# Performance work log

Measured on AMD Instinct MI355X. Metric: run time of the kernel, lower is better.

The kernel has to match this reference:

```python
import jax, jax.numpy as jnp
import numpy as np

D_MODEL = 768
N_HEADS = 4
D_HEAD = D_MODEL // N_HEADS
EPS = 1e-3  # keras LayerNormalization default


def gelu_tanh(x):
    return 0.5 * x * (1.0 + jnp.tanh(np.sqrt(2.0 / np.pi) * (x + 0.044715 * x ** 3)))


def layer_norm(x, g, b):
    mu = jnp.mean(x, axis=-1, keepdims=True)
    var = jnp.mean(jnp.square(x - mu), axis=-1, keepdims=True)
    return (x - mu) * jax.lax.rsqrt(var + EPS) * g + b


def setup_inputs() -> dict:
    key = jax.random.key(0)
    ks = jax.random.split(key, 12)
    B, S = 8, 1024
    x = jax.random.normal(ks[0], (B, S, D_MODEL), dtype=jnp.float32)
    # causal mask: 1 on strictly-future positions (added as mask * -1e9)
    mask = jnp.triu(jnp.ones((S, S), dtype=jnp.float32), k=1)[None, None]
    s = 0.02
    params = {
        'W1': jax.random.normal(ks[1], (D_MODEL, 3 * D_MODEL)) * s,
        'b1': jnp.zeros((3 * D_MODEL,), jnp.float32),
        'W3': jax.random.normal(ks[2], (D_MODEL, D_MODEL)) * s,
        'b3': jnp.zeros((D_MODEL,), jnp.float32),
        'W2': jax.random.normal(ks[3], (D_MODEL, 4 * D_MODEL)) * s,
        'b2': jnp.zeros((4 * D_MODEL,), jnp.float32),
        'W4': jax.random.normal(ks[4], (4 * D_MODEL, D_MODEL)) * s,
        'b4': jnp.zeros((D_MODEL,), jnp.float32),
        'g1': jnp.ones((D_MODEL,), jnp.float32),
        'be1': jnp.zeros((D_MODEL,), jnp.float32),
        'g2': jnp.ones((D_MODEL,), jnp.float32),
        'be2': jnp.zeros((D_MODEL,), jnp.float32),
    }
    return {'x': x, 'mask': mask, **params}


def reference(x, mask, W1, b1, W3, b3, W2, b2, W4, b4, g1, be1, g2, be2):
    B, S, _ = x.shape
    xn = layer_norm(x, g1, be1)
    qkv = xn @ W1 + b1                                  # [B,S,3D]
    q, k, v = jnp.split(qkv, 3, axis=-1)
    def split_heads(t):
        return t.reshape(B, S, N_HEADS, D_HEAD).transpose(0, 2, 1, 3)  # [B,H,S,dh]
    q, k, v = map(split_heads, (q, k, v))
    present = jnp.stack([k, v], axis=1)                  # [B,2,H,S,dh]
    w = jnp.einsum('bhqd,bhkd->bhqk', q, k)
    # NOTE: source divides by rsqrt(d_head) => multiplies by sqrt(d_head) (faithful bug)
    w = w * jnp.sqrt(jnp.float32(D_HEAD))
    w = w + mask * -1e9
    w = jax.nn.softmax(w, axis=-1)
    attn = jnp.einsum('bhqk,bhkd->bhqd', w, v)           # [B,H,S,dh]
    attn = attn.transpose(0, 2, 1, 3).reshape(B, S, D_MODEL)
    x = attn @ W3 + b3 + x                               # residual 1
    xn2 = layer_norm(x, g2, be2)
    h = gelu_tanh(xn2 @ W2 + b2)                         # [B,S,4D]
    x = h @ W4 + b4 + x                                  # residual 2
    return x, present
```

## Files before the change

### kernel.cpp

```cpp
#include <hip/hip_runtime.h>
#include <hip/hip_bf16.h>
#include <cstdint>

#define D_MODEL 768
#define NH 4
#define DH 192
#define SEQ 1024
#define BATCH 8

typedef __bf16 bf16x8 __attribute__((ext_vector_type(8)));
typedef float floatx4 __attribute__((ext_vector_type(4)));

__device__ __forceinline__ float bf2f(ushort u) {
    union { uint32_t i; float f; } x; x.i = ((uint32_t)u) << 16; return x.f;
}
__device__ __forceinline__ ushort f2bf(float f) {
    union { float f; uint32_t i; } x; x.f = f;
    uint32_t i = x.i;
    uint32_t r = (i + 0x7FFFu + ((i >> 16) & 1u)) >> 16;
    return (ushort)r;
}

template <int SPLIT>
__global__ void ln_kernel(const float* __restrict__ x, const float* __restrict__ g,
                          const float* __restrict__ be,
                          ushort* __restrict__ y_hi, ushort* __restrict__ y_lo) {
    int row = blockIdx.x;
    int tid = threadIdx.x;
    const float* xr = x + (size_t)row * D_MODEL;
    float v[3];
    float s = 0.f, ss = 0.f;
#pragma unroll
    for (int i = 0; i < 3; i++) {
        float t = xr[tid + i * 256];
        v[i] = t; s += t; ss += t * t;
    }
#pragma unroll
    for (int off = 32; off > 0; off >>= 1) {
        s += __shfl_down(s, off);
        ss += __shfl_down(ss, off);
    }
    __shared__ float rs[4], rss[4];
    int wid = tid >> 6;
    if ((tid & 63) == 0) { rs[wid] = s; rss[wid] = ss; }
    __syncthreads();
    s = rs[0] + rs[1] + rs[2] + rs[3];
    ss = rss[0] + rss[1] + rss[2] + rss[3];
    float mu = s * (1.f / 768.f);
    float var = ss * (1.f / 768.f) - mu * mu;
    float rstd = rsqrtf(var + 1e-3f);
#pragma unroll
    for (int i = 0; i < 3; i++) {
        int d = tid + i * 256;
        float val = (v[i] - mu) * rstd * g[d] + be[d];
        ushort hi = f2bf(val);
        y_hi[(size_t)row * D_MODEL + d] = hi;
        if (SPLIT) y_lo[(size_t)row * D_MODEL + d] = f2bf(val - bf2f(hi));
    }
}

__global__ void transpose_kernel(const float* __restrict__ W, ushort* __restrict__ Wt,
                                 int K, int N) {
    __shared__ ushort tile[64][65];
    int nt = N >> 6;
    int bk = blockIdx.x / nt, bn = blockIdx.x % nt;
    int tid = threadIdx.x;
#pragma unroll
    for (int i = 0; i < 16; i++) {
        int lin = i * 256 + tid; int r = lin >> 6, c = lin & 63;
        tile[r][c] = f2bf(W[(size_t)(bk * 64 + r) * N + bn * 64 + c]);
    }
    __syncthreads();
#pragma unroll
    for (int i = 0; i < 16; i++) {
        int lin = i * 256 + tid; int r = lin >> 6, c = lin & 63;
        Wt[(size_t)(bn * 64 + r) * K + bk * 64 + c] = tile[c][r];
    }
}

__global__ void transpose_split_kernel(const float* __restrict__ W,
                                       ushort* __restrict__ Wt_hi, ushort* __restrict__ Wt_lo,
                                       int K, int N) {
    __shared__ ushort th[64][65];
    __shared__ ushort tl[64][65];
    int nt = N >> 6;
    int bk = blockIdx.x / nt, bn = blockIdx.x % nt;
    int tid = threadIdx.x;
#pragma unroll
    for (int i = 0; i < 16; i++) {
        int lin = i * 256 + tid; int r = lin >> 6, c = lin & 63;
        float v = W[(size_t)(bk * 64 + r) * N + bn * 64 + c];
        ushort hi = f2bf(v);
        th[r][c] = hi;
        tl[r][c] = f2bf(v - bf2f(hi));
    }
    __syncthreads();
#pragma unroll
    for (int i = 0; i < 16; i++) {
        int lin = i * 256 + tid; int r = lin >> 6, c = lin & 63;
        size_t o = (size_t)(bn * 64 + r) * K + bk * 64 + c;
        Wt_hi[o] = th[c][r];
        Wt_lo[o] = tl[c][r];
    }
}

__global__ void transpose_v_kernel(const float* __restrict__ qkv, ushort* __restrict__ Vtg) {
    __shared__ ushort tile[64][65];
    int bi = blockIdx.x;
    int dt = bi % 12;
    int st = (bi / 12) % 16;
    int b  = bi / 192;
    int tid = threadIdx.x;
#pragma unroll
    for (int i = 0; i < 16; i++) {
        int lin = i * 256 + tid; int r = lin >> 6, c = lin & 63;
        tile[r][c] = f2bf(qkv[(size_t)(b * 1024 + st * 64 + r) * 2304 + 1536 + dt * 64 + c]);
    }
    __syncthreads();
#pragma unroll
    for (int i = 0; i < 16; i++) {
        int lin = i * 256 + tid; int r = lin >> 6, c = lin & 63;
        Vtg[(size_t)(b * 768 + dt * 64 + r) * 1024 + st * 64 + c] = tile[c][r];
    }
}

__global__ __launch_bounds__(256, 2) void gemm_qkv_split(
    const ushort* __restrict__ Ah, const ushort* __restrict__ Al,
    const ushort* __restrict__ Bh, const ushort* __restrict__ Bl,
    const float* __restrict__ bias, float* __restrict__ Cout, int M, int N, int K) {
    __shared__ __align__(16) __bf16 sAh[128][48];
    __shared__ __align__(16) __bf16 sAl[128][48];
    __shared__ __align__(16) __bf16 sBh[128][48];
    __shared__ __align__(16) __bf16 sBl[128][48];
    int tid = threadIdx.x;
    int rowBase = blockIdx.y << 7;
    int colBase = blockIdx.x << 7;
    int wave = tid >> 6, lane = tid & 63;
    int wm = (wave & 1) << 6, wn = (wave >> 1) << 6;
    int lrow = lane & 15, lk = (lane >> 4) << 3;
    floatx4 acc[4][4] = {};

    int lr = tid >> 2;
    int lc = (tid & 3) << 3;
    size_t aoff = (size_t)(rowBase + lr) * K + lc;
    size_t boff = (size_t)(colBase + lr) * K + lc;

    for (int k0 = 0; k0 < K; k0 += 32) {
        uint4 ah0 = *(const uint4*)(Ah + aoff + k0);
        uint4 ah1 = *(const uint4*)(Ah + aoff + (size_t)64 * K + k0);
        uint4 al0 = *(const uint4*)(Al + aoff + k0);
        uint4 al1 = *(const uint4*)(Al + aoff + (size_t)64 * K + k0);
        uint4 bh0 = *(const uint4*)(Bh + boff + k0);
        uint4 bh1 = *(const uint4*)(Bh + boff + (size_t)64 * K + k0);
        uint4 bl0 = *(const uint4*)(Bl + boff + k0);
        uint4 bl1 = *(const uint4*)(Bl + boff + (size_t)64 * K + k0);
        *(uint4*)&sAh[lr][lc] = ah0;  *(uint4*)&sAh[lr + 64][lc] = ah1;
        *(uint4*)&sAl[lr][lc] = al0;  *(uint4*)&sAl[lr + 64][lc] = al1;
        *(uint4*)&sBh[lr][lc] = bh0;  *(uint4*)&sBh[lr + 64][lc] = bh1;
        *(uint4*)&sBl[lr][lc] = bl0;  *(uint4*)&sBl[lr + 64][lc] = bl1;
        __syncthreads();
        bf16x8 afh[4], afl[4], bvh[4], bvl[4];
#pragma unroll
        for (int i = 0; i < 4; i++) {
            afh[i] = *(const bf16x8*)&sAh[wm + i * 16 + lrow][lk];
            afl[i] = *(const bf16x8*)&sAl[wm + i * 16 + lrow][lk];
        }
#pragma unroll
        for (int jj = 0; jj < 4; jj++) {
            bvh[jj] = *(const bf16x8*)&sBh[wn + jj * 16 + lrow][lk];
            bvl[jj] = *(const bf16x8*)&sBl[wn + jj * 16 + lrow][lk];
        }
#pragma unroll
        for (int i = 0; i < 4; i++)
#pragma unroll
            for (int jj = 0; jj < 4; jj++) {
                acc[i][jj] = __builtin_amdgcn_mfma_f32_16x16x32_bf16(afh[i], bvh[jj], acc[i][jj], 0, 0, 0);
                acc[i][jj] = __builtin_amdgcn_mfma_f32_16x16x32_bf16(afh[i], bvl[jj], acc[i][jj], 0, 0, 0);
                acc[i][jj] = __builtin_amdgcn_mfma_f32_16x16x32_bf16(afl[i], bvh[jj], acc[i][jj], 0, 0, 0);
            }
        __syncthreads();
    }
    int cr = (lane >> 4) << 2;
    int cc = lane & 15;
#pragma unroll
    for (int jj = 0; jj < 4; jj++) {
        int col = colBase + wn + jj * 16 + cc;
        float bvs = bias[col];
#pragma unroll
        for (int i = 0; i < 4; i++) {
            int row0 = rowBase + wm + i * 16 + cr;
#pragma unroll
            for (int r = 0; r < 4; r++)
                Cout[(size_t)(row0 + r) * N + col] = acc[i][jj][r] + bvs;
        }
    }
}

template <int GELU, int RES, int OUTF32>
__global__ __launch_bounds__(256, 2) void gemm_bt(
    const ushort* __restrict__ A, const ushort* __restrict__ Bt,
    const float* __restrict__ bias, const float* __restrict__ resid,
    void* __restrict__ Cout, int M, int N, int K) {
    __shared__ __align__(16) __bf16 sA[128][48];
    __shared__ __align__(16) __bf16 sB[128][48];
    int tid = threadIdx.x;
    int rowBase = blockIdx.y << 7;
    int colBase = blockIdx.x << 7;
    int wave = tid >> 6, lane = tid & 63;
    int wm = (wave & 1) << 6, wn = (wave >> 1) << 6;
    int lrow = lane & 15, lk = (lane >> 4) << 3;
    floatx4 acc[4][4] = {};

    int lr = tid >> 2;
    int lc = (tid & 3) << 3;
    const ushort* Ab = A + (size_t)(rowBase + lr) * K + lc;
    const ushort* Bb = Bt + (size_t)(colBase + lr) * K + lc;

    for (int k0 = 0; k0 < K; k0 += 32) {
        uint4 a0 = *(const uint4*)(Ab + k0);
        uint4 a1 = *(const uint4*)(Ab + (size_t)64 * K + k0);
        uint4 b0 = *(const uint4*)(Bb + k0);
        uint4 b1 = *(const uint4*)(Bb + (size_t)64 * K + k0);
        *(uint4*)&sA[lr][lc] = a0;
        *(uint4*)&sA[lr + 64][lc] = a1;
        *(uint4*)&sB[lr][lc] = b0;
        *(uint4*)&sB[lr + 64][lc] = b1;
        __syncthreads();
        bf16x8 af[4], bv[4];
#pragma unroll
        for (int i = 0; i < 4; i++) af[i] = *(const bf16x8*)&sA[wm + i * 16 + lrow][lk];
#pragma unroll
        for (int jj = 0; jj < 4; jj++) bv[jj] = *(const bf16x8*)&sB[wn + jj * 16 + lrow][lk];
#pragma unroll
        for (int i = 0; i < 4; i++)
#pragma unroll
            for (int jj = 0; jj < 4; jj++)
                acc[i][jj] = __builtin_amdgcn_mfma_f32_16x16x32_bf16(af[i], bv[jj], acc[i][jj], 0, 0, 0);
        __syncthreads();
    }
    int cr = (lane >> 4) << 2;
    int cc = lane & 15;
#pragma unroll
    for (int jj = 0; jj < 4; jj++) {
        int col = colBase + wn + jj * 16 + cc;
        float bvs = bias[col];
#pragma unroll
        for (int i = 0; i < 4; i++) {
            int row0 = rowBase + wm + i * 16 + cr;
#pragma unroll
            for (int r = 0; r < 4; r++) {
                int row = row0 + r;
                float v = acc[i][jj][r] + bvs;
                if (GELU) {
                    float u = v;
                    v = 0.5f * u * (1.f + tanhf(0.7978845608028654f * (u + 0.044715f * u * u * u)));
                }
                if (RES) v += resid[(size_t)row * N + col];
                if (OUTF32) ((float*)Cout)[(size_t)row * N + col] = v;
                else ((ushort*)Cout)[(size_t)row * N + col] = f2bf(v);
            }
        }
    }
}

__global__ void split_kernel(const float* __restrict__ qkv, float* __restrict__ present,
                             ushort* __restrict__ Khg, ushort* __restrict__ Klg) {
    int tok = blockIdx.x;
    int tid = threadIdx.x;
    int b = tok >> 10, s = tok & 1023;
    const float* src = qkv + (size_t)tok * 2304 + 768;
#pragma unroll
    for (int i = 0; i < 6; i++) {
        int c = tid + i * 256;
        float v = src[c];
        int kv = (c >= 768) ? 1 : 0;
        int within = c - kv * 768;
        int h = within / DH;
        int d = within - h * DH;
        size_t idx = ((size_t)(((b * 2 + kv) * NH + h) * SEQ + s)) * DH + d;
        present[idx] = v;
        if (!kv) {
            ushort hi = f2bf(v);
            Khg[(size_t)tok * 768 + c] = hi;
            Klg[(size_t)tok * 768 + c] = f2bf(v - bf2f(hi));
        }
    }
}

__global__ __launch_bounds__(512, 2) void attn_flash(
    const float* __restrict__ qkv, const ushort* __restrict__ Khg,
    const ushort* __restrict__ Klg, const ushort* __restrict__ Vtg,
    ushort* __restrict__ attn2) {
    int bi = blockIdx.x;
    int j = bi & 7;
    int h = (bi >> 3) & 3;
    int b = bi >> 5;
    int tid = threadIdx.x;
    int wave = tid >> 6, lane = tid & 63;
    int l15 = lane & 15, quad = lane >> 4;
    int tile = (wave < 4) ? (15 - j) : j;
    int w16 = wave & 3;
    int s0 = tile << 6;
    int its = 2 * (15 - j) + 2;
    int myKt = (s0 + w16 * 16 + 15) >> 5;

    __shared__ __align__(16) __bf16 sKh[2][32][200];
    __shared__ __align__(16) __bf16 sKl[2][32][200];
    __shared__ __align__(16) __bf16 sVt[2][192][40];
    __shared__ __align__(16) ushort sP[8][16][40];

    const bool lo_half = (tid < 256);
    const int kr0 = tid / 24, ke0 = (tid % 24) * 8;
    const int c1 = lo_half ? (512 + tid) : (256 + tid);
    const int kr1 = c1 / 24, ke1 = (c1 % 24) * 8;
    const int vd0 = tid >> 2, ve0 = (tid & 3) * 8;
    const int vd1 = (512 + tid) >> 2, ve1 = ((512 + tid) & 3) * 8;

    const ushort* Khb = Khg + (size_t)(b * 1024) * 768 + h * 192;
    const ushort* Klb = Klg + (size_t)(b * 1024) * 768 + h * 192;
    const ushort* Vtb = Vtg + ((size_t)(b * 768) + h * 192) * 1024;
    const ushort* Bb = lo_half ? Khb : Klb;
    __bf16* pKB = lo_half ? &sKh[0][kr1][ke1] : &sKl[0][kr1][ke1];

    uint4 rA, rB, rC, rD, rE;

    rA = *(const uint4*)(Khb + (size_t)kr0 * 768 + ke0);
    rC = *(const uint4*)(Klb + (size_t)kr0 * 768 + ke0);
    rB = *(const uint4*)(Bb + (size_t)kr1 * 768 + ke1);
    rD = *(const uint4*)(Vtb + (size_t)vd0 * 1024 + ve0);
    if (lo_half) rE = *(const uint4*)(Vtb + (size_t)vd1 * 1024 + ve1);

    bf16x8 qh[6], ql[6];
    {
        int qrow = s0 + w16 * 16 + l15;
        const float* qp = qkv + (size_t)(b * SEQ + qrow) * 2304 + h * DH + quad * 8;
#pragma unroll
        for (int dt = 0; dt < 6; dt++) {
            float4 v0 = *(const float4*)(qp + dt * 32);
            float4 v1 = *(const float4*)(qp + dt * 32 + 4);
            float vv[8] = {v0.x, v0.y, v0.z, v0.w, v1.x, v1.y, v1.z, v1.w};
            bf16x8 hh, ll;
#pragma unroll
            for (int jj = 0; jj < 8; jj++) {
                float sv = vv[jj] * 13.856406460551018f;
                ushort hu = f2bf(sv);
                ((ushort*)&hh)[jj] = hu;
                ((ushort*)&ll)[jj] = f2bf(sv - bf2f(hu));
            }
            qh[dt] = hh; ql[dt] = ll;
        }
    }

    floatx4 O[12] = {};
    float m_run[4], l_run[4];
#pragma unroll
    for (int r = 0; r < 4; r++) { m_run[r] = -1e30f; l_run[r] = 0.f; }

    *(uint4*)&sKh[0][kr0][ke0] = rA;
    *(uint4*)&sKl[0][kr0][ke0] = rC;
    *(uint4*)(pKB) = rB;
    *(uint4*)&sVt[0][vd0][ve0] = rD;
    if (lo_half) *(uint4*)&sVt[0][vd1][ve1] = rE;
    __syncthreads();

    for (int kt = 0; kt < its; kt++) {
        int cur = kt & 1;
        bool pfetch = (kt + 1 < its);
        if (pfetch) {
            int koff = (kt + 1) * 32;
            rA = *(const uint4*)(Khb + (size_t)(koff + kr0) * 768 + ke0);
            rC = *(const uint4*)(Klb + (size_t)(koff + kr0) * 768 + ke0);
            rB = *(const uint4*)(Bb + (size_t)(koff + kr1) * 768 + ke1);
            rD = *(const uint4*)(Vtb + (size_t)vd0 * 1024 + koff + ve0);
            if (lo_half) rE = *(const uint4*)(Vtb + (size_t)vd1 * 1024 + koff + ve1);
        }
        if (kt <= myKt) {
            floatx4 S0 = {}, S1 = {};
#pragma unroll
            for (int dt = 0; dt < 6; dt++) {
                bf16x8 k0h = *(const bf16x8*)&sKh[cur][l15][dt * 32 + quad * 8];
                bf16x8 k0l = *(const bf16x8*)&sKl[cur][l15][dt * 32 + quad * 8];
                bf16x8 k1h = *(const bf16x8*)&sKh[cur][16 + l15][dt * 32 + quad * 8];
                bf16x8 k1l = *(const bf16x8*)&sKl[cur][16 + l15][dt * 32 + quad * 8];
                S0 = __builtin_amdgcn_mfma_f32_16x16x32_bf16(qh[dt], k0h, S0, 0, 0, 0);
                S0 = __builtin_amdgcn_mfma_f32_16x16x32_bf16(qh[dt], k0l, S0, 0, 0, 0);
                S0 = __builtin_amdgcn_mfma_f32_16x16x32_bf16(ql[dt], k0h, S0, 0, 0, 0);
                S1 = __builtin_amdgcn_mfma_f32_16x16x32_bf16(qh[dt], k1h, S1, 0, 0, 0);
                S1 = __builtin_amdgcn_mfma_f32_16x16x32_bf16(qh[dt], k1l, S1, 0, 0, 0);
                S1 = __builtin_amdgcn_mfma_f32_16x16x32_bf16(ql[dt], k1h, S1, 0, 0, 0);
            }
            int qg = s0 + w16 * 16 + quad * 4;
            int colb = kt * 32 + l15;
            float mt[4];
#pragma unroll
            for (int r = 0; r < 4; r++) {
                float a = (colb <= qg + r) ? S0[r] : -1e30f;
                float c = (colb + 16 <= qg + r) ? S1[r] : -1e30f;
                S0[r] = a; S1[r] = c;
                mt[r] = fmaxf(a, c);
            }
#pragma unroll
            for (int m = 1; m <= 8; m <<= 1)
#pragma unroll
                for (int r = 0; r < 4; r++) mt[r] = fmaxf(mt[r], __shfl_xor(mt[r], m));
            float alpha[4], rsum[4], P0[4], P1[4];
#pragma unroll
            for (int r = 0; r < 4; r++) {
                float mn = fmaxf(m_run[r], mt[r]);
                alpha[r] = __expf(m_run[r] - mn);
                m_run[r] = mn;
                P0[r] = __expf(S0[r] - mn);
                P1[r] = __expf(S1[r] - mn);
                rsum[r] = P0[r] + P1[r];
            }
#pragma unroll
            for (int m = 1; m <= 8; m <<= 1)
#pragma unroll
                for (int r = 0; r < 4; r++) rsum[r] += __shfl_xor(rsum[r], m);
#pragma unroll
            for (int r = 0; r < 4; r++) l_run[r] = l_run[r] * alpha[r] + rsum[r];
#pragma unroll
            for (int t = 0; t < 12; t++)
#pragma unroll
                for (int r = 0; r < 4; r++) O[t][r] *= alpha[r];
#pragma unroll
            for (int r = 0; r < 4; r++) {
                sP[wave][quad * 4 + r][l15]      = f2bf(P0[r]);
                sP[wave][quad * 4 + r][16 + l15] = f2bf(P1[r]);
            }
            bf16x8 pfrag = *(const bf16x8*)&sP[wave][l15][quad * 8];
#pragma unroll
            for (int t = 0; t < 12; t++) {
                bf16x8 vf = *(const bf16x8*)&sVt[cur][t * 16 + l15][quad * 8];
                O[t] = __builtin_amdgcn_mfma_f32_16x16x32_bf16(pfrag, vf, O[t], 0, 0, 0);
            }
        }
        if (pfetch) {
            int nb = cur ^ 1;
            *(uint4*)&sKh[nb][kr0][ke0] = rA;
            *(uint4*)&sKl[nb][kr0][ke0] = rC;
            *(uint4*)(pKB + nb * 6400) = rB;
            *(uint4*)&sVt[nb][vd0][ve0] = rD;
            if (lo_half) *(uint4*)&sVt[nb][vd1][ve1] = rE;
        }
        __syncthreads();
    }

    float inv[4];
#pragma unroll
    for (int r = 0; r < 4; r++) inv[r] = 1.f / l_run[r];
    int qrow = s0 + w16 * 16 + quad * 4;
#pragma unroll
    for (int t = 0; t < 12; t++)
#pragma unroll
        for (int r = 0; r < 4; r++)
            attn2[(size_t)(b * SEQ + qrow + r) * D_MODEL + h * DH + t * 16 + l15] =
                f2bf(O[t][r] * inv[r]);
}

extern "C" void kernel_launch(void* const* d_in, const int* in_sizes, int n_in,
                              void* d_out, int out_size, void* d_ws, size_t ws_size,
                              hipStream_t stream) {
    const float* x  = (const float*)d_in[0];
    const float* W1 = (const float*)d_in[2];
    const float* b1 = (const float*)d_in[3];
    const float* W3 = (const float*)d_in[4];
    const float* b3 = (const float*)d_in[5];
    const float* W2 = (const float*)d_in[6];
    const float* b2 = (const float*)d_in[7];
    const float* W4 = (const float*)d_in[8];
    const float* b4 = (const float*)d_in[9];
    const float* g1 = (const float*)d_in[10];
    const float* be1 = (const float*)d_in[11];
    const float* g2 = (const float*)d_in[12];
    const float* be2 = (const float*)d_in[13];

    char* ws = (char*)d_ws;
    ushort* W1t_hi = (ushort*)(ws + 0);
    ushort* W1t_lo = (ushort*)(ws + 3538944);
    ushort* W3t    = (ushort*)(ws + 7077888);
    ushort* W2t    = (ushort*)(ws + 8257536);
    ushort* W4t    = (ushort*)(ws + 12976128);
    ushort* xn_hi  = (ushort*)(ws + 17694720);
    ushort* attn2  = (ushort*)(ws + 17694720);
    ushort* xn_lo  = (ushort*)(ws + 30277632);
    ushort* Khg    = (ushort*)(ws + 30277632);
    ushort* xn2    = (ushort*)(ws + 30277632);
    float*  x1     = (float*)(ws + 42860544);
    ushort* Klg    = (ushort*)(ws + 42860544);
    ushort* Vtg    = (ushort*)(ws + 55443456);
    float*  qkvf   = (float*)(ws + 68026368);
    ushort* hbuf   = (ushort*)(ws + 68026368);

    float* out0 = (float*)d_out;
    float* present = out0 + 6291456;

    transpose_split_kernel<<<(768 / 64) * (2304 / 64), 256, 0, stream>>>(W1, W1t_hi, W1t_lo, 768, 2304);
    transpose_kernel<<<(768 / 64) * (768 / 64), 256, 0, stream>>>(W3, W3t, 768, 768);
    transpose_kernel<<<(768 / 64) * (3072 / 64), 256, 0, stream>>>(W2, W2t, 768, 3072);
    transpose_kernel<<<(3072 / 64) * (768 / 64), 256, 0, stream>>>(W4, W4t, 3072, 768);

    ln_kernel<1><<<8192, 256, 0, stream>>>(x, g1, be1, xn_hi, xn_lo);
    gemm_qkv_split<<<dim3(2304 / 128, 8192 / 128), 256, 0, stream>>>(
        xn_hi, xn_lo, W1t_hi, W1t_lo, b1, qkvf, 8192, 2304, 768);
    split_kernel<<<8192, 256, 0, stream>>>(qkvf, present, Khg, Klg);
    transpose_v_kernel<<<1536, 256, 0, stream>>>(qkvf, Vtg);
    attn_flash<<<BATCH * NH * 8, 512, 0, stream>>>(qkvf, Khg, Klg, Vtg, attn2);
    gemm_bt<0, 1, 1><<<dim3(768 / 128, 8192 / 128), 256, 0, stream>>>(
        attn2, W3t, b3, x, x1, 8192, 768, 768);
    ln_kernel<0><<<8192, 256, 0, stream>>>(x1, g2, be2, xn2, nullptr);
    gemm_bt<1, 0, 0><<<dim3(3072 / 128, 8192 / 128), 256, 0, stream>>>(
        xn2, W2t, b2, nullptr, hbuf, 8192, 3072, 768);
    gemm_bt<0, 1, 1><<<dim3(768 / 128, 8192 / 128), 256, 0, stream>>>(
        hbuf, W4t, b4, x1, out0, 8192, 768, 3072);
}
```

Baseline: 527.4 us.

## Prefetch next K tile into registers and double-buffer LDS in GEMM kernels

Both GEMM kernels now load the next K-slice from global memory into registers before running the MFMAs on the current slice, so load latency overlaps compute. gemm_bt double-buffers its shared tiles and needs only one barrier per iteration, while gemm_qkv_split keeps a single buffer with two barriers. LDS row padding drops from 48 to 40 elements, gemm_bt's launch bounds rise to 3 blocks per CU, and GELU is rewritten as u/(1+exp(-2z)) using the fast __expf. The risks are extra register pressure under the tighter occupancy bound and small numeric differences from the fast exp.

```diff
diff --git a/kernel.cpp b/kernel.cpp
--- a/kernel.cpp
+++ b/kernel.cpp
@@ -128,10 +128,10 @@
     const ushort* __restrict__ Ah, const ushort* __restrict__ Al,
     const ushort* __restrict__ Bh, const ushort* __restrict__ Bl,
     const float* __restrict__ bias, float* __restrict__ Cout, int M, int N, int K) {
-    __shared__ __align__(16) __bf16 sAh[128][48];
-    __shared__ __align__(16) __bf16 sAl[128][48];
-    __shared__ __align__(16) __bf16 sBh[128][48];
-    __shared__ __align__(16) __bf16 sBl[128][48];
+    __shared__ __align__(16) __bf16 sAh[128][40];
+    __shared__ __align__(16) __bf16 sAl[128][40];
+    __shared__ __align__(16) __bf16 sBh[128][40];
+    __shared__ __align__(16) __bf16 sBl[128][40];
     int tid = threadIdx.x;
     int rowBase = blockIdx.y << 7;
     int colBase = blockIdx.x << 7;
@@ -145,20 +145,37 @@
     size_t aoff = (size_t)(rowBase + lr) * K + lc;
     size_t boff = (size_t)(colBase + lr) * K + lc;
 
-    for (int k0 = 0; k0 < K; k0 += 32) {
-        uint4 ah0 = *(const uint4*)(Ah + aoff + k0);
-        uint4 ah1 = *(const uint4*)(Ah + aoff + (size_t)64 * K + k0);
-        uint4 al0 = *(const uint4*)(Al + aoff + k0);
-        uint4 al1 = *(const uint4*)(Al + aoff + (size_t)64 * K + k0);
-        uint4 bh0 = *(const uint4*)(Bh + boff + k0);
-        uint4 bh1 = *(const uint4*)(Bh + boff + (size_t)64 * K + k0);
-        uint4 bl0 = *(const uint4*)(Bl + boff + k0);
-        uint4 bl1 = *(const uint4*)(Bl + boff + (size_t)64 * K + k0);
+    {
+        uint4 ah0 = *(const uint4*)(Ah + aoff);
+        uint4 ah1 = *(const uint4*)(Ah + aoff + (size_t)64 * K);
+        uint4 al0 = *(const uint4*)(Al + aoff);
+        uint4 al1 = *(const uint4*)(Al + aoff + (size_t)64 * K);
+        uint4 bh0 = *(const uint4*)(Bh + boff);
+        uint4 bh1 = *(const uint4*)(Bh + boff + (size_t)64 * K);
+        uint4 bl0 = *(const uint4*)(Bl + boff);
+        uint4 bl1 = *(const uint4*)(Bl + boff + (size_t)64 * K);
         *(uint4*)&sAh[lr][lc] = ah0;  *(uint4*)&sAh[lr + 64][lc] = ah1;
         *(uint4*)&sAl[lr][lc] = al0;  *(uint4*)&sAl[lr + 64][lc] = al1;
         *(uint4*)&sBh[lr][lc] = bh0;  *(uint4*)&sBh[lr + 64][lc] = bh1;
         *(uint4*)&sBl[lr][lc] = bl0;  *(uint4*)&sBl[lr + 64][lc] = bl1;
-        __syncthreads();
+    }
+    __syncthreads();
+
+    int nt = K >> 5;
+    for (int t = 0; t < nt; t++) {
+        bool pf = (t + 1 < nt);
+        uint4 ah0, ah1, al0, al1, bh0, bh1, bl0, bl1;
+        if (pf) {
+            int k0 = (t + 1) << 5;
+            ah0 = *(const uint4*)(Ah + aoff + k0);
+            ah1 = *(const uint4*)(Ah + aoff + (size_t)64 * K + k0);
+            al0 = *(const uint4*)(Al + aoff + k0);
+            al1 = *(const uint4*)(Al + aoff + (size_t)64 * K + k0);
+            bh0 = *(const uint4*)(Bh + boff + k0);
+            bh1 = *(const uint4*)(Bh + boff + (size_t)64 * K + k0);
+            bl0 = *(const uint4*)(Bl + boff + k0);
+            bl1 = *(const uint4*)(Bl + boff + (size_t)64 * K + k0);
+        }
         bf16x8 afh[4], afl[4], bvh[4], bvl[4];
 #pragma unroll
         for (int i = 0; i < 4; i++) {
@@ -178,7 +195,14 @@
                 acc[i][jj] = __builtin_amdgcn_mfma_f32_16x16x32_bf16(afh[i], bvl[jj], acc[i][jj], 0, 0, 0);
                 acc[i][jj] = __builtin_amdgcn_mfma_f32_16x16x32_bf16(afl[i], bvh[jj], acc[i][jj], 0, 0, 0);
             }
-        __syncthreads();
+        if (pf) {
+            __syncthreads();
+            *(uint4*)&sAh[lr][lc] = ah0;  *(uint4*)&sAh[lr + 64][lc] = ah1;
+            *(uint4*)&sAl[lr][lc] = al0;  *(uint4*)&sAl[lr + 64][lc] = al1;
+            *(uint4*)&sBh[lr][lc] = bh0;  *(uint4*)&sBh[lr + 64][lc] = bh1;
+            *(uint4*)&sBl[lr][lc] = bl0;  *(uint4*)&sBl[lr + 64][lc] = bl1;
+            __syncthreads();
+        }
     }
     int cr = (lane >> 4) << 2;
     int cc = lane & 15;
@@ -197,12 +221,12 @@
 }
 
 template <int GELU, int RES, int OUTF32>
-__global__ __launch_bounds__(256, 2) void gemm_bt(
+__global__ __launch_bounds__(256, 3) void gemm_bt(
     const ushort* __restrict__ A, const ushort* __restrict__ Bt,
     const float* __restrict__ bias, const float* __restrict__ resid,
     void* __restrict__ Cout, int M, int N, int K) {
-    __shared__ __align__(16) __bf16 sA[128][48];
-    __shared__ __align__(16) __bf16 sB[128][48];
+    __shared__ __align__(16) __bf16 sA[2][128][40];
+    __shared__ __align__(16) __bf16 sB[2][128][40];
     int tid = threadIdx.x;
     int rowBase = blockIdx.y << 7;
     int colBase = blockIdx.x << 7;
@@ -216,26 +240,47 @@
     const ushort* Ab = A + (size_t)(rowBase + lr) * K + lc;
     const ushort* Bb = Bt + (size_t)(colBase + lr) * K + lc;
 
-    for (int k0 = 0; k0 < K; k0 += 32) {
-        uint4 a0 = *(const uint4*)(Ab + k0);
-        uint4 a1 = *(const uint4*)(Ab + (size_t)64 * K + k0);
-        uint4 b0 = *(const uint4*)(Bb + k0);
-        uint4 b1 = *(const uint4*)(Bb + (size_t)64 * K + k0);
-        *(uint4*)&sA[lr][lc] = a0;
-        *(uint4*)&sA[lr + 64][lc] = a1;
-        *(uint4*)&sB[lr][lc] = b0;
-        *(uint4*)&sB[lr + 64][lc] = b1;
-        __syncthreads();
+    {
+        uint4 a0 = *(const uint4*)(Ab);
+        uint4 a1 = *(const uint4*)(Ab + (size_t)64 * K);
+        uint4 b0 = *(const uint4*)(Bb);
+        uint4 b1 = *(const uint4*)(Bb + (size_t)64 * K);
+        *(uint4*)&sA[0][lr][lc] = a0;
+        *(uint4*)&sA[0][lr + 64][lc] = a1;
+        *(uint4*)&sB[0][lr][lc] = b0;
+        *(uint4*)&sB[0][lr + 64][lc] = b1;
+    }
+    __syncthreads();
+
+    int nt = K >> 5;
+    for (int t = 0; t < nt; t++) {
+        int cur = t & 1;
+        bool pf = (t + 1 < nt);
+        uint4 a0, a1, b0, b1;
+        if (pf) {
+            int k0 = (t + 1) << 5;
+            a0 = *(const uint4*)(Ab + k0);
+            a1 = *(const uint4*)(Ab + (size_t)64 * K + k0);
+            b0 = *(const uint4*)(Bb + k0);
+            b1 = *(const uint4*)(Bb + (size_t)64 * K + k0);
+        }
         bf16x8 af[4], bv[4];
 #pragma unroll
-        for (int i = 0; i < 4; i++) af[i] = *(const bf16x8*)&sA[wm + i * 16 + lrow][lk];
-#pragma unroll
-        for (int jj = 0; jj < 4; jj++) bv[jj] = *(const bf16x8*)&sB[wn + jj * 16 + lrow][lk];
+        for (int i = 0; i < 4; i++) af[i] = *(const bf16x8*)&sA[cur][wm + i * 16 + lrow][lk];
+#pragma unroll
+        for (int jj = 0; jj < 4; jj++) bv[jj] = *(const bf16x8*)&sB[cur][wn + jj * 16 + lrow][lk];
 #pragma unroll
         for (int i = 0; i < 4; i++)
 #pragma unroll
             for (int jj = 0; jj < 4; jj++)
                 acc[i][jj] = __builtin_amdgcn_mfma_f32_16x16x32_bf16(af[i], bv[jj], acc[i][jj], 0, 0, 0);
+        if (pf) {
+            int nb = cur ^ 1;
+            *(uint4*)&sA[nb][lr][lc] = a0;
+            *(uint4*)&sA[nb][lr + 64][lc] = a1;
+            *(uint4*)&sB[nb][lr][lc] = b0;
+            *(uint4*)&sB[nb][lr + 64][lc] = b1;
+        }
         __syncthreads();
     }
     int cr = (lane >> 4) << 2;
@@ -253,7 +298,8 @@
                 float v = acc[i][jj][r] + bvs;
                 if (GELU) {
                     float u = v;
-                    v = 0.5f * u * (1.f + tanhf(0.7978845608028654f * (u + 0.044715f * u * u * u)));
+                    float z2 = -1.5957691216057308f * (u + 0.044715f * u * u * u);
+                    v = u / (1.f + __expf(z2));
                 }
                 if (RES) v += resid[(size_t)row * N + col];
                 if (OUTF32) ((float*)Cout)[(size_t)row * N + col] = v;
```

New measurement: 520.9 us. About the same (-1.2%).
